# Performance work log

Measured on AMD Instinct MI355X. Metric: run time of the kernel, lower is better.

The kernel has to match this reference:

```python
import jax, jax.numpy as jnp
import numpy as np

EPS = 1e-5

def _conv1x1(x, w, b):
    # x: (b,c,t,h,w), w: (o,c), b: (o,)  -> (b,o,t,h,w)
    return jnp.einsum('bcthw,oc->bothw', x, w) + b[None, :, None, None, None]

def setup_inputs() -> dict:
    key = jax.random.key(0)
    ks = jax.random.split(key, 12)
    B, C, IC, T, H, W = 32, 1024, 512, 8, 16, 8
    s_c = 1.0 / np.sqrt(C)
    s_ic = 1.0 / np.sqrt(IC)
    return {
        'x':       jax.random.normal(ks[0], (B, C, T, H, W), jnp.float32),
        'g_w':     jax.random.normal(ks[1], (IC, C), jnp.float32) * s_c,
        'g_b':     jax.random.normal(ks[2], (IC,), jnp.float32) * 0.01,
        'theta_w': jax.random.normal(ks[3], (IC, C), jnp.float32) * s_c,
        'theta_b': jax.random.normal(ks[4], (IC,), jnp.float32) * 0.01,
        'phi_w':   jax.random.normal(ks[5], (IC, C), jnp.float32) * s_c,
        'phi_b':   jax.random.normal(ks[6], (IC,), jnp.float32) * 0.01,
        'w_w':     jax.random.normal(ks[7], (C, IC), jnp.float32) * s_ic,
        'w_b':     jax.random.normal(ks[8], (C,), jnp.float32) * 0.01,
        'bn_gamma': jax.random.normal(ks[9], (C,), jnp.float32) * 0.1 + 1.0,
        'bn_beta':  jax.random.normal(ks[10], (C,), jnp.float32) * 0.01,
        'bn_mean':  jax.random.normal(ks[11], (C,), jnp.float32) * 0.01,
        'bn_var':   jnp.ones((C,), jnp.float32),
    }

def reference(x, g_w, g_b, theta_w, theta_b, phi_w, phi_b, w_w, w_b,
              bn_gamma, bn_beta, bn_mean, bn_var):
    B, C, T, H, W = x.shape
    IC = g_w.shape[0]
    # value projection, flattened per frame: (b, t, ic*h*w)
    g_x = _conv1x1(x, g_w, g_b)                       # (b,ic,t,h,w)
    g_x = jnp.transpose(g_x, (0, 2, 1, 3, 4)).reshape(B, T, IC * H * W)
    # pooled query/key over spatial dims: (b,t,ic) and (b,ic,t)
    theta = _conv1x1(x, theta_w, theta_b).mean(axis=(3, 4))   # (b,ic,t)
    phi = _conv1x1(x, phi_w, phi_b).mean(axis=(3, 4))         # (b,ic,t)
    f = jnp.einsum('bct,bcs->bts', theta, phi)                # (b,t,t)
    attn = jax.nn.softmax(f, axis=-1)
    y = jnp.einsum('bts,bsd->btd', attn, g_x)                 # (b,t,ic*h*w)
    y = jnp.transpose(y.reshape(B, T, IC, H, W), (0, 2, 1, 3, 4))  # (b,ic,t,h,w)
    # output projection + BatchNorm3d (inference stats) + residual
    wy = _conv1x1(y, w_w, w_b)                        # (b,c,t,h,w)
    inv = bn_gamma / jnp.sqrt(bn_var + EPS)
    wy = wy * inv[None, :, None, None, None] + (bn_beta - bn_mean * inv)[None, :, None, None, None]
    return wy + x
```

## Files before the change

kernel.cpp:

```cpp
#include <hip/hip_runtime.h>
#include <hip/hip_bf16.h>

typedef __attribute__((ext_vector_type(8))) short bf16x8;
typedef __attribute__((ext_vector_type(4))) float f32x4;

#if defined(__has_builtin)
#if __has_builtin(__builtin_amdgcn_global_load_lds)
#define USE_GLOAD_LDS 1
#endif
#endif

__device__ __forceinline__ void gload_lds16(const void* g, void* ldsbase) {
#ifdef USE_GLOAD_LDS
    __builtin_amdgcn_global_load_lds(
        (__attribute__((address_space(1))) void*)(g),
        (__attribute__((address_space(3))) void*)(ldsbase), 16, 0, 0);
#endif
}

__global__ __launch_bounds__(256) void early_kernel(
        const float* __restrict__ x, float* __restrict__ xbar,
        const float* __restrict__ gw, const float* __restrict__ ww,
        __hip_bfloat16* __restrict__ gwt, __hip_bfloat16* __restrict__ wwb,
        const float* __restrict__ gb, const float* __restrict__ wb,
        const float* __restrict__ gamma, const float* __restrict__ beta,
        const float* __restrict__ mean, const float* __restrict__ var,
        float* __restrict__ inv, float* __restrict__ shift) {
    __shared__ float tile[32][33];
    int bid = blockIdx.x;
    int tid = threadIdx.x;
    if (bid < 16384) {
        int row = bid * 16 + (tid >> 4);
        int j = tid & 15;
        const float4* p = (const float4*)(x + (size_t)row * 128);
        float4 a = p[j * 2], b2 = p[j * 2 + 1];
        float s = a.x + a.y + a.z + a.w + b2.x + b2.y + b2.z + b2.w;
        s += __shfl_xor(s, 1); s += __shfl_xor(s, 2);
        s += __shfl_xor(s, 4); s += __shfl_xor(s, 8);
        if (j == 0) xbar[row] = s * (1.0f / 128.0f);
    } else if (bid < 16896) {
        int b2 = bid - 16384;
        int icb = b2 >> 5, cb = b2 & 31;
        int r = tid >> 5, c = tid & 31;
        #pragma unroll
        for (int i = 0; i < 4; i++)
            tile[r + i * 8][c] = gw[(size_t)(icb * 32 + r + i * 8) * 1024 + cb * 32 + c];
        __syncthreads();
        #pragma unroll
        for (int i = 0; i < 4; i++) {
            int cin = cb * 32 + r + i * 8;
            gwt[(size_t)cin * 512 + icb * 32 + c] = __float2bfloat16(tile[c][r + i * 8]);
        }
    } else if (bid < 17152) {
        int b2 = bid - 16896;
        size_t base = (size_t)b2 * 2048 + (size_t)tid * 8;
        const float4* src = (const float4*)(ww + base);
        float4 v0 = src[0], v1 = src[1];
        __hip_bfloat16 tmp[8];
        tmp[0] = __float2bfloat16(v0.x); tmp[1] = __float2bfloat16(v0.y);
        tmp[2] = __float2bfloat16(v0.z); tmp[3] = __float2bfloat16(v0.w);
        tmp[4] = __float2bfloat16(v1.x); tmp[5] = __float2bfloat16(v1.y);
        tmp[6] = __float2bfloat16(v1.z); tmp[7] = __float2bfloat16(v1.w);
        *(bf16x8*)(wwb + base) = *(const bf16x8*)tmp;
    } else {
        int b2 = bid - 17152;
        int wv = tid >> 6, l = tid & 63;
        int c = b2 * 32 + wv * 8 + (l >> 3);
        int j = l & 7;
        const float* wr = ww + (size_t)c * 512;
        float acc = 0.0f;
        #pragma unroll 8
        for (int k = j; k < 512; k += 8) acc += wr[k] * gb[k];
        acc += __shfl_xor(acc, 1); acc += __shfl_xor(acc, 2); acc += __shfl_xor(acc, 4);
        if (j == 0) {
            float cb2 = wb[c] + acc;
            float iv = gamma[c] * rsqrtf(var[c] + 1e-5f);
            inv[c] = iv;
            shift[c] = cb2 * iv + beta[c] - mean[c] * iv;
        }
    }
}

__global__ __launch_bounds__(256) void stage2_kernel(
        const float* __restrict__ xbar,
        const float* __restrict__ tw, const float* __restrict__ tb,
        const float* __restrict__ pw, const float* __restrict__ pb,
        float* __restrict__ theta, float* __restrict__ phi,
        const __hip_bfloat16* __restrict__ wwb,
        const __hip_bfloat16* __restrict__ gwt,
        __hip_bfloat16* __restrict__ M) {
    __shared__ __align__(16) char smem[32768];
    int bid = blockIdx.x;
    int tid = threadIdx.x;
    if (bid < 1024) {
        float* xs = (float*)smem;
        int which = bid & 1;
        int icc = (bid >> 1) & 15;
        int b = bid >> 5;
        const float* w = which ? pw : tw;
        const float* bias = which ? pb : tb;
        float* out = which ? phi : theta;
        for (int i = tid; i < 8192; i += 256) xs[i] = xbar[b * 8192 + i];
        __syncthreads();
        int icl = tid >> 3;
        int t = tid & 7;
        int ic = icc * 32 + icl;
        const float* wr = w + (size_t)ic * 1024;
        float acc = 0.0f;
        #pragma unroll 8
        for (int k = 0; k < 1024; k++) acc += wr[k] * xs[k * 8 + t];
        out[((size_t)b * 512 + ic) * 8 + t] = acc + bias[ic];
    } else {
        __hip_bfloat16* As = (__hip_bfloat16*)smem;
        __hip_bfloat16* Bs = (__hip_bfloat16*)(smem + 8192);
        int b2 = bid - 1024;
        int mb = b2 >> 3, nb = b2 & 7;
        int c0 = mb * 128, n0 = nb * 128;
        int w = tid >> 6, l = tid & 63;
        int wr = w >> 1, wc = w & 1;
        const __hip_bfloat16* Ab = wwb + (size_t)c0 * 512;
        const __hip_bfloat16* Bb = gwt + (size_t)n0 * 512;
        int arow = tid >> 2, akq = tid & 3;
        f32x4 acc[4][4] = {};
        for (int kk = 0; kk < 16; ++kk) {
            int k0 = kk * 32;
#ifdef USE_GLOAD_LDS
            gload_lds16(Ab + (size_t)arow * 512 + k0 + akq * 8,        (char*)As + w * 1024);
            gload_lds16(Ab + (size_t)(arow + 64) * 512 + k0 + akq * 8, (char*)As + 4096 + w * 1024);
            gload_lds16(Bb + (size_t)arow * 512 + k0 + akq * 8,        (char*)Bs + w * 1024);
            gload_lds16(Bb + (size_t)(arow + 64) * 512 + k0 + akq * 8, (char*)Bs + 4096 + w * 1024);
#else
            *(bf16x8*)((char*)As + (size_t)tid * 16)        = *(const bf16x8*)(Ab + (size_t)arow * 512 + k0 + akq * 8);
            *(bf16x8*)((char*)As + 4096 + (size_t)tid * 16) = *(const bf16x8*)(Ab + (size_t)(arow + 64) * 512 + k0 + akq * 8);
            *(bf16x8*)((char*)Bs + (size_t)tid * 16)        = *(const bf16x8*)(Bb + (size_t)arow * 512 + k0 + akq * 8);
            *(bf16x8*)((char*)Bs + 4096 + (size_t)tid * 16) = *(const bf16x8*)(Bb + (size_t)(arow + 64) * 512 + k0 + akq * 8);
#endif
            __syncthreads();
            const __hip_bfloat16* Ap = As + ((size_t)(wr * 64 + (l & 15)) * 32) + (l >> 4) * 8;
            const __hip_bfloat16* Bp = Bs + ((size_t)(wc * 64 + (l & 15)) * 32) + (l >> 4) * 8;
            bf16x8 af[4], bfr[4];
            #pragma unroll
            for (int m = 0; m < 4; m++) af[m] = *(const bf16x8*)(Ap + m * 16 * 32);
            #pragma unroll
            for (int n = 0; n < 4; n++) bfr[n] = *(const bf16x8*)(Bp + n * 16 * 32);
            #pragma unroll
            for (int m = 0; m < 4; m++)
                #pragma unroll
                for (int n = 0; n < 4; n++)
                    acc[m][n] = __builtin_amdgcn_mfma_f32_16x16x32_bf16(af[m], bfr[n], acc[m][n], 0, 0, 0);
            __syncthreads();
        }
        int col = l & 15, rg = l >> 4;
        #pragma unroll
        for (int m = 0; m < 4; m++)
            #pragma unroll
            for (int j = 0; j < 4; j++) {
                int gc = c0 + wr * 64 + m * 16 + rg * 4 + j;
                #pragma unroll
                for (int n = 0; n < 4; n++)
                    M[(size_t)gc * 1024 + n0 + wc * 64 + n * 16 + col] = __float2bfloat16(acc[m][n][j]);
            }
    }
}

__global__ __launch_bounds__(64) void attn_kernel(const float* __restrict__ theta,
                                                  const float* __restrict__ phi,
                                                  float* __restrict__ attn) {
    __shared__ float th[4096], ph[4096];
    int b = blockIdx.x, lane = threadIdx.x;
    for (int i = lane; i < 4096; i += 64) {
        th[i] = theta[(size_t)b * 4096 + i];
        ph[i] = phi[(size_t)b * 4096 + i];
    }
    __syncthreads();
    int t = lane >> 3, s = lane & 7;
    float f = 0.0f;
    #pragma unroll 8
    for (int ic = 0; ic < 512; ic++) f += th[ic * 8 + t] * ph[ic * 8 + s];
    float m = f;
    m = fmaxf(m, __shfl_xor(m, 1));
    m = fmaxf(m, __shfl_xor(m, 2));
    m = fmaxf(m, __shfl_xor(m, 4));
    float e = __expf(f - m);
    float sum = e;
    sum += __shfl_xor(sum, 1); sum += __shfl_xor(sum, 2); sum += __shfl_xor(sum, 4);
    attn[b * 64 + lane] = e / sum;
}

__global__ __launch_bounds__(256) void mix_kernel(const float* __restrict__ x,
                                                  const float* __restrict__ attn,
                                                  __hip_bfloat16* __restrict__ xmt) {
    int orig = blockIdx.x;
    int wg = (orig & 7) * 64 + (orig >> 3);
    int b = wg >> 4;
    int hwg = wg & 15;
    __shared__ float at[64];
    __shared__ float xs[8][8][33];
    int tid = threadIdx.x;
    if (tid < 64) at[tid] = attn[b * 64 + tid];
    int ci = tid >> 3, s = tid & 7;
    int h = tid >> 5, cq = tid & 31;
    const float* xb = x + ((size_t)b << 20);
    __hip_bfloat16* ob = xmt + ((size_t)b << 20);
    for (int cc = 0; cc < 32; ++cc) {
        const float4* src = (const float4*)(xb + ((size_t)(cc * 32 + ci) * 8 + s) * 128 + hwg * 8);
        float4 v0 = src[0], v1 = src[1];
        __syncthreads();
        xs[s][0][ci] = v0.x; xs[s][1][ci] = v0.y; xs[s][2][ci] = v0.z; xs[s][3][ci] = v0.w;
        xs[s][4][ci] = v1.x; xs[s][5][ci] = v1.y; xs[s][6][ci] = v1.z; xs[s][7][ci] = v1.w;
        __syncthreads();
        float xr[8];
        #pragma unroll
        for (int ss = 0; ss < 8; ss++) xr[ss] = xs[ss][h][cq];
        #pragma unroll
        for (int t = 0; t < 8; t++) {
            float o = 0.0f;
            #pragma unroll
            for (int ss = 0; ss < 8; ss++) o += at[t * 8 + ss] * xr[ss];
            ob[(size_t)(t * 128 + hwg * 8 + h) * 1024 + cc * 32 + cq] = __float2bfloat16(o);
        }
    }
}

__global__ __launch_bounds__(512, 2) void gemm256_kernel(
        const __hip_bfloat16* __restrict__ Mw,
        const __hip_bfloat16* __restrict__ xmt,
        const float* __restrict__ x,
        const float* __restrict__ inv, const float* __restrict__ shift,
        float* __restrict__ out) {
    __shared__ __align__(16) __hip_bfloat16 HBs[65536];
    char* AH = (char*)HBs;
    const int BUFB = 32768;

    int orig = blockIdx.x;
    int bid = (orig & 7) * 64 + (orig >> 3);
    int b = bid >> 4;
    int mb = (bid >> 2) & 3;
    int nb = bid & 3;
    int c0 = mb * 256, n0 = nb * 256;

    int tid = threadIdx.x;
    int w = tid >> 6, l = tid & 63;
    int wr = w >> 2, wc = w & 3;

    int sgl = (((l & 3) - ((l >> 3) & 3)) & 3);
    const __hip_bfloat16* aS = Mw + (size_t)(c0 + w * 16 + (l >> 2)) * 1024 + sgl * 8;
    const __hip_bfloat16* bS = xmt + ((size_t)b << 20) + (size_t)(n0 + w * 16 + (l >> 2)) * 1024 + sgl * 8;
    int stBase = w * 1024;

    int rdSlot = ((l >> 4) + (((l & 15) >> 1) & 3)) & 3;
    int aRdBase = (wr * 128 + (l & 15)) * 64 + rdSlot * 16;
    int bRdBase = 16384 + (wc * 64 + (l & 15)) * 64 + rdSlot * 16;

    f32x4 acc[8][4] = {};

    #define ISSUE(q3) do {                                                      \
        gload_lds16(aS,              AH + (q3) * BUFB + stBase);                \
        gload_lds16(aS + 128 * 1024, AH + (q3) * BUFB + stBase + 8192);         \
        gload_lds16(bS,              AH + (q3) * BUFB + 16384 + stBase);        \
        gload_lds16(bS + 128 * 1024, AH + (q3) * BUFB + 16384 + stBase + 8192); \
        aS += 32; bS += 32;                                                     \
    } while (0)

    #define V8 asm volatile("s_waitcnt vmcnt(8)" ::: "memory")
    #define V4 asm volatile("s_waitcnt vmcnt(4)" ::: "memory")
    #define V0 asm volatile("s_waitcnt vmcnt(0)" ::: "memory")

    #define HSTEP(q, DOISS, WAITM, LAST) do {                                   \
        if (DOISS) ISSUE(((q) + 3) & 3);                                        \
        const char* bufA = AH + (q) * BUFB;                                     \
        bf16x8 bfr[4];                                                          \
        _Pragma("unroll")                                                       \
        for (int n = 0; n < 4; ++n)                                             \
            bfr[n] = *(const bf16x8*)(bufA + bRdBase + n * 1024);               \
        __builtin_amdgcn_s_setprio(1);                                          \
        _Pragma("unroll")                                                       \
        for (int mi = 0; mi < 8; ++mi) {                                        \
            bf16x8 af = *(const bf16x8*)(bufA + aRdBase + mi * 1024);           \
            _Pragma("unroll")                                                   \
            for (int n = 0; n < 4; ++n)                                         \
                acc[mi][n] = __builtin_amdgcn_mfma_f32_16x16x32_bf16(           \
                    af, bfr[n], acc[mi][n], 0, 0, 0);                           \
        }                                                                       \
        __builtin_amdgcn_s_setprio(0);                                          \
        if (!LAST) {                                                            \
            WAITM;                                                              \
            __builtin_amdgcn_s_barrier();                                       \
            __builtin_amdgcn_sched_barrier(0);                                  \
        }                                                                       \
    } while (0)

    ISSUE(0); ISSUE(1); ISSUE(2);
    V8;
    __builtin_amdgcn_s_barrier();
    __builtin_amdgcn_sched_barrier(0);

    #pragma unroll 1
    for (int t = 0; t < 7; ++t) {
        HSTEP(0, 1, V8, 0);
        HSTEP(1, 1, V8, 0);
        HSTEP(2, 1, V8, 0);
        HSTEP(3, 1, V8, 0);
    }
    HSTEP(0, 1, V8, 0);
    HSTEP(1, 0, V4, 0);
    HSTEP(2, 0, V0, 0);
    HSTEP(3, 0, V0, 1);

    #undef ISSUE
    #undef HSTEP
    #undef V8
    #undef V4
    #undef V0

    int col = l & 15, rg = l >> 4;
    const float* xb = x + ((size_t)b << 20);
    float* ob = out + ((size_t)b << 20);
    #pragma unroll
    for (int mi = 0; mi < 8; ++mi) {
        #pragma unroll
        for (int j = 0; j < 4; ++j) {
            int gc = c0 + wr * 128 + mi * 16 + rg * 4 + j;
            float iv = inv[gc], sh = shift[gc];
            size_t rowoff = (size_t)gc * 1024 + n0 + wc * 64 + col;
            #pragma unroll
            for (int n = 0; n < 4; ++n) {
                size_t idx = rowoff + n * 16;
                ob[idx] = acc[mi][n][j] * iv + sh + xb[idx];
            }
        }
    }
}

extern "C" void kernel_launch(void* const* d_in, const int* in_sizes, int n_in,
                              void* d_out, int out_size, void* d_ws, size_t ws_size,
                              hipStream_t stream) {
    const float* x    = (const float*)d_in[0];
    const float* g_w  = (const float*)d_in[1];
    const float* g_b  = (const float*)d_in[2];
    const float* th_w = (const float*)d_in[3];
    const float* th_b = (const float*)d_in[4];
    const float* ph_w = (const float*)d_in[5];
    const float* ph_b = (const float*)d_in[6];
    const float* w_w  = (const float*)d_in[7];
    const float* w_b  = (const float*)d_in[8];
    const float* gam  = (const float*)d_in[9];
    const float* bet  = (const float*)d_in[10];
    const float* mea  = (const float*)d_in[11];
    const float* var  = (const float*)d_in[12];
    float* out = (float*)d_out;
    char* ws = (char*)d_ws;

    __hip_bfloat16* xmt = (__hip_bfloat16*)ws;
    __hip_bfloat16* Mw  = (__hip_bfloat16*)(ws + 67108864);
    float* xbar  = (float*)(ws + 69206016);
    float* theta = (float*)(ws + 70254592);
    float* phi   = (float*)(ws + 70778880);
    float* attn  = (float*)(ws + 71303168);
    float* inv   = (float*)(ws + 71311360);
    float* shift = (float*)(ws + 71315456);
    __hip_bfloat16* gwt = (__hip_bfloat16*)ws;
    __hip_bfloat16* wwb = (__hip_bfloat16*)(ws + 1048576);

    hipLaunchKernelGGL(early_kernel, dim3(17184), dim3(256), 0, stream,
                       x, xbar, g_w, w_w, gwt, wwb,
                       g_b, w_b, gam, bet, mea, var, inv, shift);
    hipLaunchKernelGGL(stage2_kernel, dim3(1088), dim3(256), 0, stream,
                       xbar, th_w, th_b, ph_w, ph_b, theta, phi, wwb, gwt, Mw);
    hipLaunchKernelGGL(attn_kernel, dim3(32), dim3(64), 0, stream, theta, phi, attn);
    hipLaunchKernelGGL(mix_kernel, dim3(512), dim3(256), 0, stream, x, attn, xmt);
    hipLaunchKernelGGL(gemm256_kernel, dim3(512), dim3(512), 0, stream,
                       Mw, xmt, x, inv, shift, out);
}
```

Baseline: 236.7 us.

## Split GEMM k-step into two barrier-synchronized phases with explicit LDS waits

```diff
diff --git a/kernel.cpp b/kernel.cpp
--- a/kernel.cpp
+++ b/kernel.cpp
@@ -253,6 +253,7 @@
     int bRdBase = 16384 + (wc * 64 + (l & 15)) * 64 + rdSlot * 16;
 
     f32x4 acc[8][4] = {};
+    bf16x8 bfr[4];
 
     #define ISSUE(q3) do {                                                      \
         gload_lds16(aS,              AH + (q3) * BUFB + stBase);                \
@@ -265,53 +266,78 @@
     #define V8 asm volatile("s_waitcnt vmcnt(8)" ::: "memory")
     #define V4 asm volatile("s_waitcnt vmcnt(4)" ::: "memory")
     #define V0 asm volatile("s_waitcnt vmcnt(0)" ::: "memory")
-
-    #define HSTEP(q, DOISS, WAITM, LAST) do {                                   \
-        if (DOISS) ISSUE(((q) + 3) & 3);                                        \
-        const char* bufA = AH + (q) * BUFB;                                     \
-        bf16x8 bfr[4];                                                          \
+    #define VN ((void)0)
+    #define SB0 __builtin_amdgcn_sched_barrier(0)
+    #define BAR __builtin_amdgcn_s_barrier()
+    #define LGKM0 asm volatile("s_waitcnt lgkmcnt(0)" ::: "memory")
+
+    #define PH_LO(q, DOISS, ibuf) do {                                          \
+        const char* bp = AH + (q) * BUFB;                                       \
         _Pragma("unroll")                                                       \
         for (int n = 0; n < 4; ++n)                                             \
-            bfr[n] = *(const bf16x8*)(bufA + bRdBase + n * 1024);               \
+            bfr[n] = *(const bf16x8*)(bp + bRdBase + n * 1024);                 \
+        bf16x8 af0, af1, af2, af3;                                              \
+        af0 = *(const bf16x8*)(bp + aRdBase);                                   \
+        af1 = *(const bf16x8*)(bp + aRdBase + 1024);                            \
+        af2 = *(const bf16x8*)(bp + aRdBase + 2048);                            \
+        af3 = *(const bf16x8*)(bp + aRdBase + 3072);                            \
+        if (DOISS) ISSUE(ibuf);                                                 \
+        SB0; BAR; LGKM0; SB0;                                                   \
         __builtin_amdgcn_s_setprio(1);                                          \
         _Pragma("unroll")                                                       \
-        for (int mi = 0; mi < 8; ++mi) {                                        \
-            bf16x8 af = *(const bf16x8*)(bufA + aRdBase + mi * 1024);           \
-            _Pragma("unroll")                                                   \
-            for (int n = 0; n < 4; ++n)                                         \
-                acc[mi][n] = __builtin_amdgcn_mfma_f32_16x16x32_bf16(           \
-                    af, bfr[n], acc[mi][n], 0, 0, 0);                           \
+        for (int n = 0; n < 4; ++n) {                                           \
+            acc[0][n] = __builtin_amdgcn_mfma_f32_16x16x32_bf16(af0, bfr[n], acc[0][n], 0, 0, 0); \
+            acc[1][n] = __builtin_amdgcn_mfma_f32_16x16x32_bf16(af1, bfr[n], acc[1][n], 0, 0, 0); \
+            acc[2][n] = __builtin_amdgcn_mfma_f32_16x16x32_bf16(af2, bfr[n], acc[2][n], 0, 0, 0); \
+            acc[3][n] = __builtin_amdgcn_mfma_f32_16x16x32_bf16(af3, bfr[n], acc[3][n], 0, 0, 0); \
         }                                                                       \
         __builtin_amdgcn_s_setprio(0);                                          \
-        if (!LAST) {                                                            \
-            WAITM;                                                              \
-            __builtin_amdgcn_s_barrier();                                       \
-            __builtin_amdgcn_sched_barrier(0);                                  \
+        SB0; BAR;                                                               \
+    } while (0)
+
+    #define PH_HI(q, WAITM, LAST) do {                                          \
+        const char* bp = AH + (q) * BUFB;                                       \
+        bf16x8 af4, af5, af6, af7;                                              \
+        af4 = *(const bf16x8*)(bp + aRdBase + 4096);                            \
+        af5 = *(const bf16x8*)(bp + aRdBase + 5120);                            \
+        af6 = *(const bf16x8*)(bp + aRdBase + 6144);                            \
+        af7 = *(const bf16x8*)(bp + aRdBase + 7168);                            \
+        SB0; BAR; LGKM0; SB0;                                                   \
+        __builtin_amdgcn_s_setprio(1);                                          \
+        _Pragma("unroll")                                                       \
+        for (int n = 0; n < 4; ++n) {                                           \
+            acc[4][n] = __builtin_amdgcn_mfma_f32_16x16x32_bf16(af4, bfr[n], acc[4][n], 0, 0, 0); \
+            acc[5][n] = __builtin_amdgcn_mfma_f32_16x16x32_bf16(af5, bfr[n], acc[5][n], 0, 0, 0); \
+            acc[6][n] = __builtin_amdgcn_mfma_f32_16x16x32_bf16(af6, bfr[n], acc[6][n], 0, 0, 0); \
+            acc[7][n] = __builtin_amdgcn_mfma_f32_16x16x32_bf16(af7, bfr[n], acc[7][n], 0, 0, 0); \
         }                                                                       \
+        __builtin_amdgcn_s_setprio(0);                                          \
+        SB0; WAITM;                                                             \
+        if (!(LAST)) { BAR; }                                                   \
     } while (0)
 
     ISSUE(0); ISSUE(1); ISSUE(2);
     V8;
-    __builtin_amdgcn_s_barrier();
-    __builtin_amdgcn_sched_barrier(0);
+    BAR; SB0;
 
     #pragma unroll 1
-    for (int t = 0; t < 7; ++t) {
-        HSTEP(0, 1, V8, 0);
-        HSTEP(1, 1, V8, 0);
-        HSTEP(2, 1, V8, 0);
-        HSTEP(3, 1, V8, 0);
-    }
-    HSTEP(0, 1, V8, 0);
-    HSTEP(1, 0, V4, 0);
-    HSTEP(2, 0, V0, 0);
-    HSTEP(3, 0, V0, 1);
+    for (int t2 = 0; t2 < 7; ++t2) {
+        PH_LO(0, 1, 3); PH_HI(0, V8, 0); PH_LO(1, 1, 0); PH_HI(1, V8, 0);
+        PH_LO(2, 1, 1); PH_HI(2, V8, 0); PH_LO(3, 1, 2); PH_HI(3, V8, 0);
+    }
+    PH_LO(0, 1, 3); PH_HI(0, V8, 0); PH_LO(1, 0, 0); PH_HI(1, V4, 0);
+    PH_LO(2, 0, 0); PH_HI(2, V0, 0); PH_LO(3, 0, 0); PH_HI(3, VN, 1);
 
     #undef ISSUE
-    #undef HSTEP
+    #undef PH_LO
+    #undef PH_HI
     #undef V8
     #undef V4
     #undef V0
+    #undef VN
+    #undef SB0
+    #undef BAR
+    #undef LGKM0
 
     int col = l & 15, rg = l >> 4;
     const float* xb = x + ((size_t)b << 20);
```

Result: no change. 240.5 us (+1.6%).

## Shrink final GEMM to 128x128 tiles with double-buffered LDS pipeline

Applied to the files above, without the earlier changes.

```diff
diff --git a/kernel.cpp b/kernel.cpp
--- a/kernel.cpp
+++ b/kernel.cpp
@@ -222,26 +222,26 @@
     }
 }
 
-__global__ __launch_bounds__(512, 2) void gemm256_kernel(
+__global__ __launch_bounds__(256, 3) void gemm128_kernel(
         const __hip_bfloat16* __restrict__ Mw,
         const __hip_bfloat16* __restrict__ xmt,
         const float* __restrict__ x,
         const float* __restrict__ inv, const float* __restrict__ shift,
         float* __restrict__ out) {
-    __shared__ __align__(16) __hip_bfloat16 HBs[65536];
+    __shared__ __align__(16) __hip_bfloat16 HBs[16384];
     char* AH = (char*)HBs;
-    const int BUFB = 32768;
+    const int BUFB = 16384;
 
     int orig = blockIdx.x;
-    int bid = (orig & 7) * 64 + (orig >> 3);
-    int b = bid >> 4;
-    int mb = (bid >> 2) & 3;
-    int nb = bid & 3;
-    int c0 = mb * 256, n0 = nb * 256;
+    int bid = (orig & 7) * 256 + (orig >> 3);
+    int b = bid >> 6;
+    int mb = (bid >> 3) & 7;
+    int nb = bid & 7;
+    int c0 = mb * 128, n0 = nb * 128;
 
     int tid = threadIdx.x;
     int w = tid >> 6, l = tid & 63;
-    int wr = w >> 2, wc = w & 3;
+    int wr = w >> 1, wc = w & 1;
 
     int sgl = (((l & 3) - ((l >> 3) & 3)) & 3);
     const __hip_bfloat16* aS = Mw + (size_t)(c0 + w * 16 + (l >> 2)) * 1024 + sgl * 8;
@@ -249,78 +249,81 @@
     int stBase = w * 1024;
 
     int rdSlot = ((l >> 4) + (((l & 15) >> 1) & 3)) & 3;
-    int aRdBase = (wr * 128 + (l & 15)) * 64 + rdSlot * 16;
-    int bRdBase = 16384 + (wc * 64 + (l & 15)) * 64 + rdSlot * 16;
-
-    f32x4 acc[8][4] = {};
-
-    #define ISSUE(q3) do {                                                      \
-        gload_lds16(aS,              AH + (q3) * BUFB + stBase);                \
-        gload_lds16(aS + 128 * 1024, AH + (q3) * BUFB + stBase + 8192);         \
-        gload_lds16(bS,              AH + (q3) * BUFB + 16384 + stBase);        \
-        gload_lds16(bS + 128 * 1024, AH + (q3) * BUFB + 16384 + stBase + 8192); \
+    int aRdBase = (wr * 64 + (l & 15)) * 64 + rdSlot * 16;
+    int bRdBase = 8192 + (wc * 64 + (l & 15)) * 64 + rdSlot * 16;
+
+    f32x4 acc[4][4] = {};
+
+    #define ISSUE(q) do {                                                       \
+        gload_lds16(aS,             AH + (q) * BUFB + stBase);                  \
+        gload_lds16(aS + 64 * 1024, AH + (q) * BUFB + 4096 + stBase);           \
+        gload_lds16(bS,             AH + (q) * BUFB + 8192 + stBase);           \
+        gload_lds16(bS + 64 * 1024, AH + (q) * BUFB + 12288 + stBase);          \
         aS += 32; bS += 32;                                                     \
     } while (0)
 
-    #define V8 asm volatile("s_waitcnt vmcnt(8)" ::: "memory")
     #define V4 asm volatile("s_waitcnt vmcnt(4)" ::: "memory")
     #define V0 asm volatile("s_waitcnt vmcnt(0)" ::: "memory")
-
-    #define HSTEP(q, DOISS, WAITM, LAST) do {                                   \
-        if (DOISS) ISSUE(((q) + 3) & 3);                                        \
-        const char* bufA = AH + (q) * BUFB;                                     \
-        bf16x8 bfr[4];                                                          \
-        _Pragma("unroll")                                                       \
-        for (int n = 0; n < 4; ++n)                                             \
-            bfr[n] = *(const bf16x8*)(bufA + bRdBase + n * 1024);               \
+    #define SB0 __builtin_amdgcn_sched_barrier(0)
+    #define BAR __builtin_amdgcn_s_barrier()
+    #define LGKM0 asm volatile("s_waitcnt lgkmcnt(0)" ::: "memory")
+
+    #define HSTEP(q, MODE) do {                                                 \
+        const char* bp = AH + (q) * BUFB;                                       \
+        bf16x8 af0 = *(const bf16x8*)(bp + aRdBase);                            \
+        bf16x8 af1 = *(const bf16x8*)(bp + aRdBase + 1024);                     \
+        bf16x8 af2 = *(const bf16x8*)(bp + aRdBase + 2048);                     \
+        bf16x8 af3 = *(const bf16x8*)(bp + aRdBase + 3072);                     \
+        bf16x8 bf0 = *(const bf16x8*)(bp + bRdBase);                            \
+        bf16x8 bf1 = *(const bf16x8*)(bp + bRdBase + 1024);                     \
+        bf16x8 bf2 = *(const bf16x8*)(bp + bRdBase + 2048);                     \
+        bf16x8 bf3 = *(const bf16x8*)(bp + bRdBase + 3072);                     \
+        LGKM0; SB0;                                                             \
+        BAR;                                  \
+        if ((MODE) == 0) ISSUE(q);              \
+        SB0;                                                                    \
         __builtin_amdgcn_s_setprio(1);                                          \
         _Pragma("unroll")                                                       \
-        for (int mi = 0; mi < 8; ++mi) {                                        \
-            bf16x8 af = *(const bf16x8*)(bufA + aRdBase + mi * 1024);           \
-            _Pragma("unroll")                                                   \
-            for (int n = 0; n < 4; ++n)                                         \
-                acc[mi][n] = __builtin_amdgcn_mfma_f32_16x16x32_bf16(           \
-                    af, bfr[n], acc[mi][n], 0, 0, 0);                           \
+        for (int n = 0; n < 4; ++n) {                                           \
+            bf16x8 bfn = (n == 0) ? bf0 : (n == 1) ? bf1 : (n == 2) ? bf2 : bf3;\
+            acc[0][n] = __builtin_amdgcn_mfma_f32_16x16x32_bf16(af0, bfn, acc[0][n], 0, 0, 0); \
+            acc[1][n] = __builtin_amdgcn_mfma_f32_16x16x32_bf16(af1, bfn, acc[1][n], 0, 0, 0); \
+            acc[2][n] = __builtin_amdgcn_mfma_f32_16x16x32_bf16(af2, bfn, acc[2][n], 0, 0, 0); \
+            acc[3][n] = __builtin_amdgcn_mfma_f32_16x16x32_bf16(af3, bfn, acc[3][n], 0, 0, 0); \
         }                                                                       \
         __builtin_amdgcn_s_setprio(0);                                          \
-        if (!LAST) {                                                            \
-            WAITM;                                                              \
-            __builtin_amdgcn_s_barrier();                                       \
-            __builtin_amdgcn_sched_barrier(0);                                  \
-        }                                                                       \
+        SB0;                                                                    \
+        if ((MODE) == 0) { V4; BAR; SB0; }                                      \
+        else if ((MODE) == 1) { V0; BAR; SB0; }                                 \
     } while (0)
 
-    ISSUE(0); ISSUE(1); ISSUE(2);
-    V8;
-    __builtin_amdgcn_s_barrier();
-    __builtin_amdgcn_sched_barrier(0);
+    ISSUE(0); ISSUE(1);
+    V4; BAR; SB0;
 
     #pragma unroll 1
-    for (int t = 0; t < 7; ++t) {
-        HSTEP(0, 1, V8, 0);
-        HSTEP(1, 1, V8, 0);
-        HSTEP(2, 1, V8, 0);
-        HSTEP(3, 1, V8, 0);
-    }
-    HSTEP(0, 1, V8, 0);
-    HSTEP(1, 0, V4, 0);
-    HSTEP(2, 0, V0, 0);
-    HSTEP(3, 0, V0, 1);
+    for (int t = 0; t < 15; ++t) {
+        HSTEP(0, 0);
+        HSTEP(1, 0);
+    }
+    HSTEP(0, 1);
+    HSTEP(1, 2);
 
     #undef ISSUE
     #undef HSTEP
-    #undef V8
     #undef V4
     #undef V0
+    #undef SB0
+    #undef BAR
+    #undef LGKM0
 
     int col = l & 15, rg = l >> 4;
     const float* xb = x + ((size_t)b << 20);
     float* ob = out + ((size_t)b << 20);
     #pragma unroll
-    for (int mi = 0; mi < 8; ++mi) {
+    for (int mi = 0; mi < 4; ++mi) {
         #pragma unroll
         for (int j = 0; j < 4; ++j) {
-            int gc = c0 + wr * 128 + mi * 16 + rg * 4 + j;
+            int gc = c0 + wr * 64 + mi * 16 + rg * 4 + j;
             float iv = inv[gc], sh = shift[gc];
             size_t rowoff = (size_t)gc * 1024 + n0 + wc * 64 + col;
             #pragma unroll
@@ -369,6 +372,6 @@
                        xbar, th_w, th_b, ph_w, ph_b, theta, phi, wwb, gwt, Mw);
     hipLaunchKernelGGL(attn_kernel, dim3(32), dim3(64), 0, stream, theta, phi, attn);
     hipLaunchKernelGGL(mix_kernel, dim3(512), dim3(256), 0, stream, x, attn, xmt);
-    hipLaunchKernelGGL(gemm256_kernel, dim3(512), dim3(512), 0, stream,
+    hipLaunchKernelGGL(gemm128_kernel, dim3(2048), dim3(256), 0, stream,
                        Mw, xmt, x, inv, shift, out);
 }
```

Result: no change. 233.5 us (-1.4%).
